# Performance work log

Hardware: AMD Instinct MI355X
Metric: run time of the kernel (lower is better)

## Reference

```python
import jax, jax.numpy as jnp
import numpy as np

D_MODEL = 768
N_HEADS = 8
Q_RANK = 64
KV_RANK = 64
ROPE_DIM = 64
NOPE_DIM = D_MODEL // N_HEADS - ROPE_DIM  # 32
V_DIM = D_MODEL // N_HEADS               # 96
Q_HEAD_DIM = NOPE_DIM + ROPE_DIM         # 96
EPS = 1e-6
ROPE_BASE = 10000.0


def rms_norm(x, w, eps=EPS):
    v = jnp.mean(jnp.square(x.astype(jnp.float32)), axis=-1, keepdims=True)
    return (x.astype(jnp.float32) * jax.lax.rsqrt(v + eps)).astype(x.dtype) * w


def rope_cos_sin(seq_len, dim):
    inv_freq = 1.0 / (ROPE_BASE ** (jnp.arange(0, dim, 2, dtype=jnp.float32) / dim))
    freqs = jnp.outer(jnp.arange(seq_len, dtype=jnp.float32), inv_freq)
    emb = jnp.concatenate([freqs, freqs], axis=-1)  # [s, dim]
    return jnp.cos(emb), jnp.sin(emb)


def apply_rope(x, cos, sin, pos_ids):
    # x: [b,h,s,d]; DeepSeek-V2 de-interleaves pairs before rotate_half
    b, h, s, d = x.shape
    x = x.reshape(b, h, s, d // 2, 2).transpose(0, 1, 2, 4, 3).reshape(b, h, s, d)
    c = cos[pos_ids][:, None]  # [b,1,s,d]
    sn = sin[pos_ids][:, None]
    x1, x2 = jnp.split(x, 2, axis=-1)
    rot = jnp.concatenate([-x2, x1], axis=-1)
    return x * c + rot * sn


def setup_inputs() -> dict:
    key = jax.random.key(0)
    ks = jax.random.split(key, 8)
    s = 0.02
    return {
        "src": jax.random.normal(ks[0], (4, 2048, D_MODEL), jnp.float32),
        "wq_a": jax.random.normal(ks[1], (Q_RANK, D_MODEL), jnp.float32) * s,
        "q_a_ln_w": jnp.ones((Q_RANK,), jnp.float32),
        "wq_b": jax.random.normal(ks[2], (N_HEADS * Q_HEAD_DIM, Q_RANK), jnp.float32) * s,
        "wkv_a": jax.random.normal(ks[3], (KV_RANK + ROPE_DIM, D_MODEL), jnp.float32) * s,
        "kv_a_ln_w": jnp.ones((KV_RANK,), jnp.float32),
        "wkv_b": jax.random.normal(ks[4], (N_HEADS * (NOPE_DIM + V_DIM), KV_RANK), jnp.float32) * s,
        "wo": jax.random.normal(ks[5], (D_MODEL, N_HEADS * V_DIM), jnp.float32) * s,
        "norm_w": jnp.ones((D_MODEL,), jnp.float32),
    }


def reference(src, wq_a, q_a_ln_w, wq_b, wkv_a, kv_a_ln_w, wkv_b, wo, norm_w):
    b, s, _ = src.shape
    pos = jnp.broadcast_to(jnp.arange(s)[None], (b, s))
    cos, sin = rope_cos_sin(s, ROPE_DIM)

    # ---- compress_kv (torch.no_grad in original) ----
    ckv = src @ wkv_a.T                                  # [b,s,rank+rope]
    c_lat, k_pe = ckv[..., :KV_RANK], ckv[..., KV_RANK:]
    c_lat = rms_norm(c_lat, kv_a_ln_w)
    k_pe = apply_rope(k_pe[:, None], cos, sin, pos)[:, 0]  # [b,s,rope]
    c_lat = jax.lax.stop_gradient(c_lat)
    k_pe = jax.lax.stop_gradient(k_pe)

    # ---- query path ----
    q = rms_norm(src @ wq_a.T, q_a_ln_w) @ wq_b.T        # [b,s,h*96]
    q = q.reshape(b, s, N_HEADS, Q_HEAD_DIM).transpose(0, 2, 1, 3)
    q_nope, q_pe = q[..., :NOPE_DIM], q[..., NOPE_DIM:]
    q_pe = apply_rope(q_pe, cos, sin, pos)

    # ---- absorb kv_b_proj ----
    w = wkv_b.reshape(N_HEADS, NOPE_DIM + V_DIM, KV_RANK)
    q_absorb, out_absorb = w[:, :NOPE_DIM], w[:, NOPE_DIM:]   # [h,32,r], [h,96,r]
    q_lat = jnp.einsum('bhsd,hdr->bhsr', q_nope, q_absorb)    # [b,h,s,r]

    scale = Q_HEAD_DIM ** -0.5
    scores = (jnp.einsum('bhsr,btr->bhst', q_lat, c_lat)
              + jnp.einsum('bhsd,btd->bhst', q_pe, k_pe)) * scale
    attn = jax.nn.softmax(scores.astype(jnp.float32), axis=-1).astype(src.dtype)

    ctx = jnp.einsum('bhst,btr->bhsr', attn, c_lat)           # [b,h,s,r]
    ctx = jnp.einsum('bhsr,hvr->bhsv', ctx, out_absorb)       # [b,h,s,96]
    attn_out = ctx.transpose(0, 2, 1, 3).reshape(b, s, N_HEADS * V_DIM) @ wo.T

    # residual (dropout in eval = identity) + RMSNorm
    return rms_norm(src + attn_out, norm_w)
```

## Files before the change

### kernel.cpp

```cpp
#include <hip/hip_runtime.h>


#define DEV static __device__ __forceinline__
typedef unsigned short ushort_t;
typedef __attribute__((ext_vector_type(8))) short bf8_t;
typedef __attribute__((ext_vector_type(4))) float f4_t;

DEV float bf2f(unsigned int u) {
    union { float f; unsigned int i; } x; x.i = u << 16; return x.f;
}
DEV ushort_t f2bf(float f) {
    union { float f; unsigned int u; } x; x.f = f;
    unsigned int u = x.u;
    return (ushort_t)((u + 0x7fffu + ((u >> 16) & 1u)) >> 16);
}
DEV float ldin(const void* p, size_t i, int isbf) {
    return isbf ? bf2f(((const ushort_t*)p)[i]) : ((const float*)p)[i];
}
DEV float fexp2(float x) {
#if __has_builtin(__builtin_amdgcn_exp2f)
    return __builtin_amdgcn_exp2f(x);
#else
    return exp2f(x);
#endif
}

constexpr int   TOK   = 4 * 2048;
constexpr float EPSF  = 1e-6f;
constexpr float QSCALE = (float)(0.10206207261596575 * 1.4426950408889634);
constexpr float L2_10000_OVER_32 = 0.4152410118609203f;

constexpr size_t OFF_WOT   = 0;
constexpr size_t OFF_WKVAT = 589824;
constexpr size_t OFF_WQAT  = 688128;
constexpr size_t OFF_WQBT  = 737280;
constexpr size_t OFF_QAF   = 786432;
constexpr size_t OFF_OAT   = 802816;
constexpr size_t OFF_QLN   = 851968;
constexpr size_t OFF_KVLN  = 852032;
constexpr size_t OFF_NW    = 852096;
constexpr size_t OFF_FLAG  = 852864;
constexpr size_t OFF_CTXF  = 852880;
constexpr size_t OFF_SRCBF = 3998608;
constexpr size_t OFF_KBF   = 7144336;
constexpr size_t OFF_VTB   = 7668624;
constexpr size_t OFF_QBF   = 7930768;
constexpr size_t OFF_ROPE  = 12125072;

__global__ void det_k(const unsigned int* __restrict__ nw_u, int* __restrict__ flag) {
    *flag = ((nw_u[0] & 0xffffu) != 0u) ? 1 : 0;
}

__global__ __launch_bounds__(256) void prep_k(
    const void* __restrict__ wq_a, const void* __restrict__ q_ln,
    const void* __restrict__ wq_b, const void* __restrict__ wkv_a,
    const void* __restrict__ kv_ln, const void* __restrict__ wkv_b,
    const void* __restrict__ wo, const void* __restrict__ nw,
    float* __restrict__ ws)
{
    const int isbf = ((const int*)ws)[OFF_FLAG];
    int i = blockIdx.x * 256 + threadIdx.x;
    int y = blockIdx.y;
    if (y == 0) {
        if (i < 768 * 768) {
            ushort_t* wob = (ushort_t*)(ws + OFF_WOT);
            wob[i] = isbf ? ((const ushort_t*)wo)[i] : f2bf(((const float*)wo)[i]);
        }
    } else if (y == 1) {
        if (i < 128 * 768) {
            ushort_t* d = (ushort_t*)(ws + OFF_WKVAT);
            d[i] = isbf ? ((const ushort_t*)wkv_a)[i] : f2bf(((const float*)wkv_a)[i]);
        }
    } else if (y == 2) {
        if (i < 64 * 768) {
            ushort_t* d = (ushort_t*)(ws + OFF_WQAT);
            d[i] = isbf ? ((const ushort_t*)wq_a)[i] : f2bf(((const float*)wq_a)[i]);
        }
    } else if (y == 3) {
        if (i < 768 * 64) {
            ushort_t* d = (ushort_t*)(ws + OFF_WQBT);
            d[i] = isbf ? ((const ushort_t*)wq_b)[i] : f2bf(((const float*)wq_b)[i]);
        }
    } else if (y == 4) {
        if (i < 8 * 64 * 32) {
            int h = i >> 11, rem = i & 2047, r = rem >> 5, d = rem & 31;
            ushort_t* dst = (ushort_t*)(ws + OFF_QAF);
            dst[i] = f2bf(ldin(wkv_b, (size_t)(h * 128 + d) * 64 + r, isbf) * QSCALE);
        }
    } else if (y == 5) {
        if (i < 8 * 64 * 96) {
            int h = i / 6144, rem = i - h * 6144;
            int r = rem / 96, v = rem - r * 96;
            ws[OFF_OAT + i] = ldin(wkv_b, (size_t)h * 8192 + 2048 + v * 64 + r, isbf);
        }
    } else if (y == 6) {
        if (i < 64)             ws[OFF_QLN + i]       = ldin(q_ln, i, isbf);
        else if (i < 128)       ws[OFF_KVLN + i - 64] = ldin(kv_ln, i - 64, isbf);
        else if (i < 128 + 768) ws[OFF_NW + i - 128]  = ldin(nw, i - 128, isbf);
    } else {
        if (i < 2048 * 32) {
            int pos = i >> 5, p = i & 31;
            float inv = exp2f(-(float)p * L2_10000_OVER_32);
            float ang = (float)pos * inv;
            float2* tab = (float2*)(ws + OFF_ROPE);
            tab[i] = make_float2(cosf(ang), sinf(ang));
        }
    }
}

__global__ __launch_bounds__(512) void k1_ckv(
    const void* __restrict__ src, const float* __restrict__ ws,
    ushort_t* __restrict__ Kbf, ushort_t* __restrict__ VTbf,
    ushort_t* __restrict__ srcbf)
{
    const ushort_t* wkvab = (const ushort_t*)(ws + OFF_WKVAT);
    const float* kvln  = ws + OFF_KVLN;
    const float2* tab  = (const float2*)(ws + OFF_ROPE);
    const int isbf = ((const int*)ws)[OFF_FLAG];
    __shared__ __align__(16) ushort_t sA[32 * 776];
    __shared__ float ckv[32][132];
    int j = threadIdx.x;
    int t0 = blockIdx.x * 32;
    int w = j >> 6, lane = j & 63;
    int tl = lane & 15, qd = lane >> 4;

    {
        for (int e = j; e < 32 * 96; e += 512) {
            int row = e / 96, c8 = e - row * 96;
            size_t off = (size_t)(t0 + row) * 768 + c8 * 8;
            if (isbf) {
                uint4 v = *(const uint4*)((const ushort_t*)src + off);
                *(uint4*)(sA + row * 776 + c8 * 8) = v;
            } else {
                const float4* p = (const float4*)((const float*)src + off);
                float4 f0 = p[0], f1 = p[1];
                ushort_t tmp[8] = {f2bf(f0.x), f2bf(f0.y), f2bf(f0.z), f2bf(f0.w),
                                   f2bf(f1.x), f2bf(f1.y), f2bf(f1.z), f2bf(f1.w)};
                uint4 v = *(const uint4*)tmp;
                *(uint4*)(sA + row * 776 + c8 * 8) = v;
                *(uint4*)(srcbf + off) = v;
            }
        }
    }
    __syncthreads();
    {
        f4_t acc[2];
        acc[0] = (f4_t){0.f, 0.f, 0.f, 0.f};
        acc[1] = (f4_t){0.f, 0.f, 0.f, 0.f};
        const ushort_t* bp = wkvab + (size_t)(w * 16 + tl) * 768 + qd * 8;
#pragma unroll 4
        for (int ks = 0; ks < 24; ++ks) {
            bf8_t b  = *(const bf8_t*)(bp + ks * 32);
            bf8_t a0 = *(const bf8_t*)(sA + tl * 776 + ks * 32 + qd * 8);
            bf8_t a1 = *(const bf8_t*)(sA + (16 + tl) * 776 + ks * 32 + qd * 8);
            acc[0] = __builtin_amdgcn_mfma_f32_16x16x32_bf16(a0, b, acc[0], 0, 0, 0);
            acc[1] = __builtin_amdgcn_mfma_f32_16x16x32_bf16(a1, b, acc[1], 0, 0, 0);
        }
#pragma unroll
        for (int mt = 0; mt < 2; ++mt)
#pragma unroll
            for (int r = 0; r < 4; ++r)
                ckv[mt * 16 + qd * 4 + r][w * 16 + tl] = acc[mt][r];
    }
    __syncthreads();

    if (j < 256) {
        int tt = j >> 3, l = j & 7;
        float ss = 0.f;
#pragma unroll
        for (int i = 0; i < 8; ++i) { float v = ckv[tt][l * 8 + i]; ss += v * v; }
        ss += __shfl_xor(ss, 1); ss += __shfl_xor(ss, 2); ss += __shfl_xor(ss, 4);
        float rs = rsqrtf(ss * (1.f / 64.f) + EPSF);
        size_t base = (size_t)(t0 + tt) * 128;
        ushort_t kb[8];
        float clw[8];
#pragma unroll
        for (int i = 0; i < 8; ++i) {
            int o2 = l * 8 + i;
            float cl = ckv[tt][o2] * rs;
            if (isbf) cl = bf2f(f2bf(cl));
            clw[i] = cl * kvln[o2];
            kb[i] = f2bf(clw[i]);
        }
        uint4 pack;
        pack.x = kb[0] | ((unsigned)kb[1] << 16); pack.y = kb[2] | ((unsigned)kb[3] << 16);
        pack.z = kb[4] | ((unsigned)kb[5] << 16); pack.w = kb[6] | ((unsigned)kb[7] << 16);
        *(uint4*)&Kbf[base + l * 8] = pack;
        int pos = (t0 + tt) & 2047;
        ushort_t r0[4], r1[4];
#pragma unroll
        for (int i = 0; i < 4; ++i) {
            int p = l * 4 + i;
            float2 cssn = tab[pos * 32 + p];
            float e = ckv[tt][64 + 2 * p], od = ckv[tt][64 + 2 * p + 1];
            r0[i] = f2bf(e * cssn.x - od * cssn.y);
            r1[i] = f2bf(od * cssn.x + e * cssn.y);
        }
        uint2 p0, p1;
        p0.x = r0[0] | ((unsigned)r0[1] << 16); p0.y = r0[2] | ((unsigned)r0[3] << 16);
        p1.x = r1[0] | ((unsigned)r1[1] << 16); p1.y = r1[2] | ((unsigned)r1[3] << 16);
        *(uint2*)&Kbf[base + 64 + l * 4] = p0;
        *(uint2*)&Kbf[base + 96 + l * 4] = p1;
#pragma unroll
        for (int i = 0; i < 8; ++i) ckv[tt][l * 8 + i] = clw[i];
    }
    __syncthreads();
    if (j < 256) {
        int t = j & 31, rb = (j >> 5) * 8;
        int bb = t0 >> 11, col = (t0 & 2047) + t;
#pragma unroll
        for (int i = 0; i < 8; ++i) {
            int r = rb + i;
            VTbf[((size_t)(bb * 64 + r)) * 2048 + col] = f2bf(ckv[t][r]);
        }
    }
}

__global__ __launch_bounds__(128) void k2_q(
    const void* __restrict__ src, const float* __restrict__ ws, ushort_t* __restrict__ Qbf)
{
    const int isbf = ((const int*)ws)[OFF_FLAG];
    const ushort_t* srcb = isbf ? (const ushort_t*)src : (const ushort_t*)(ws + OFF_SRCBF);
    const ushort_t* wqab = (const ushort_t*)(ws + OFF_WQAT);
    const ushort_t* wqbb = (const ushort_t*)(ws + OFF_WQBT);
    const ushort_t* qabs = (const ushort_t*)(ws + OFF_QAF);
    const float2*   tab  = (const float2*)(ws + OFF_ROPE);
    const float*    qln  = ws + OFF_QLN;

    __shared__ __align__(16) ushort_t LDS[2 * 3968];
    int j = threadIdx.x;
    int w = j >> 6, lane = j & 63;
    int tl = lane & 15, qd = lane >> 4;
    ushort_t* tmpn = LDS + w * 3968;
    ushort_t* qn   = tmpn + 1152;
    ushort_t* qf   = qn + 640;
    int tokw = blockIdx.x * 16;

    f4_t C1[4];
#pragma unroll
    for (int nt = 0; nt < 4; ++nt) C1[nt] = (f4_t){0.f, 0.f, 0.f, 0.f};
    {
        const ushort_t* ap = srcb + (size_t)(tokw + tl) * 768 + qd * 8;
#pragma unroll 4
        for (int ks = 0; ks < 24; ++ks) {
            bf8_t a = *(const bf8_t*)(ap + ks * 32);
#pragma unroll
            for (int nt = 0; nt < 4; ++nt) {
                bf8_t bfr = *(const bf8_t*)(wqab + (size_t)(nt * 16 + tl) * 768 + ks * 32 + qd * 8);
                C1[nt] = __builtin_amdgcn_mfma_f32_16x16x32_bf16(a, bfr, C1[nt], 0, 0, 0);
            }
        }
    }
    float rsv[4];
#pragma unroll
    for (int r = 0; r < 4; ++r) {
        float s = C1[0][r] * C1[0][r] + C1[1][r] * C1[1][r]
                + C1[2][r] * C1[2][r] + C1[3][r] * C1[3][r];
        s += __shfl_xor(s, 1); s += __shfl_xor(s, 2);
        s += __shfl_xor(s, 4); s += __shfl_xor(s, 8);
        rsv[r] = rsqrtf(s * (1.f / 64.f) + EPSF);
    }
    float qlnv[4];
#pragma unroll
    for (int nt = 0; nt < 4; ++nt) qlnv[nt] = qln[nt * 16 + tl];
#pragma unroll
    for (int nt = 0; nt < 4; ++nt)
#pragma unroll
        for (int r = 0; r < 4; ++r) {
            float v = C1[nt][r] * rsv[r];
            if (isbf) v = bf2f(f2bf(v));
            tmpn[(qd * 4 + r) * 72 + nt * 16 + tl] = f2bf(v * qlnv[nt]);
        }
    bf8_t A2[2];
#pragma unroll
    for (int ks = 0; ks < 2; ++ks) A2[ks] = *(const bf8_t*)(tmpn + tl * 72 + ks * 32 + qd * 8);

    float csv[4][4], snv[4][4];
#pragma unroll
    for (int nt2 = 0; nt2 < 4; ++nt2) {
        int p = (nt2 * 16 + tl) >> 1;
#pragma unroll
        for (int r = 0; r < 4; ++r) {
            int pos = (tokw + qd * 4 + r) & 2047;
            float2 t = tab[pos * 32 + p];
            csv[nt2][r] = t.x * QSCALE;
            snv[nt2][r] = t.y * QSCALE;
        }
    }
    const bool evn = !(tl & 1);
    int bb = tokw >> 11, pos0 = tokw & 2047;

    for (int h = w * 4; h < w * 4 + 4; ++h) {
        f4_t C2[6];
#pragma unroll
        for (int nt = 0; nt < 6; ++nt) C2[nt] = (f4_t){0.f, 0.f, 0.f, 0.f};
#pragma unroll
        for (int nt = 0; nt < 6; ++nt)
#pragma unroll
            for (int ks = 0; ks < 2; ++ks) {
                bf8_t bfr = *(const bf8_t*)(wqbb + (size_t)(h * 96 + nt * 16 + tl) * 64 + ks * 32 + qd * 8);
                C2[nt] = __builtin_amdgcn_mfma_f32_16x16x32_bf16(A2[ks], bfr, C2[nt], 0, 0, 0);
            }
#pragma unroll
        for (int nt = 0; nt < 2; ++nt)
#pragma unroll
            for (int r = 0; r < 4; ++r)
                qn[(qd * 4 + r) * 40 + nt * 16 + tl] = f2bf(C2[nt][r]);
        bf8_t an = *(const bf8_t*)(qn + tl * 40 + qd * 8);
        f4_t C3[4];
#pragma unroll
        for (int nt = 0; nt < 4; ++nt) C3[nt] = (f4_t){0.f, 0.f, 0.f, 0.f};
#pragma unroll
        for (int nt = 0; nt < 4; ++nt) {
            bf8_t bfr = *(const bf8_t*)(qabs + (size_t)h * 2048 + (nt * 16 + tl) * 32 + qd * 8);
            C3[nt] = __builtin_amdgcn_mfma_f32_16x16x32_bf16(an, bfr, C3[nt], 0, 0, 0);
        }
#pragma unroll
        for (int nt = 0; nt < 4; ++nt)
#pragma unroll
            for (int r = 0; r < 4; ++r)
                qf[(qd * 4 + r) * 136 + nt * 16 + tl] = f2bf(C3[nt][r]);
#pragma unroll
        for (int nt2 = 0; nt2 < 4; ++nt2) {
            int p = (nt2 * 16 + tl) >> 1;
            int outc = evn ? (64 + p) : (96 + p);
#pragma unroll
            for (int r = 0; r < 4; ++r) {
                float val = C2[nt2 + 2][r];
                float part = __shfl_xor(val, 1);
                float res = evn ? (val * csv[nt2][r] - part * snv[nt2][r])
                                : (val * csv[nt2][r] + part * snv[nt2][r]);
                qf[(qd * 4 + r) * 136 + outc] = f2bf(res);
            }
        }
        size_t qb = ((size_t)(bb * 8 + h) * 2048 + pos0) * 128;
#pragma unroll
        for (int i = 0; i < 4; ++i) {
            int idx = i * 64 + lane;
            int row = idx >> 4, c = idx & 15;
            uint4 v = *(const uint4*)(qf + row * 136 + c * 8);
            *(uint4*)(Qbf + qb + (size_t)row * 128 + c * 8) = v;
        }
    }
}

__global__ __launch_bounds__(256, 2) void k3_attn(
    const ushort_t* __restrict__ Qbf, const ushort_t* __restrict__ Kbf,
    const ushort_t* __restrict__ VTbf, const float* __restrict__ oaT,
    ushort_t* __restrict__ ctxb)
{
    __shared__ __align__(16) ushort_t LDS[22528];
    ushort_t* Kt = LDS;
    ushort_t* Vt = LDS + 8704;
    ushort_t* Pw = LDS + 13312;
    int j = threadIdx.x;
    int b = blockIdx.z, h = blockIdx.y, q0g = blockIdx.x * 128;
    int w = j >> 6, lane = j & 63;
    int tl = lane & 15, qd = lane >> 4;
    ushort_t* Pme = Pw + w * 2304;
    int qw = q0g + w * 32;

    bf8_t qfA[4], qfB[4];
    {
        const ushort_t* qp = Qbf + ((size_t)((b * 8 + h) * 2048) + qw + tl) * 128 + qd * 8;
#pragma unroll
        for (int ks = 0; ks < 4; ++ks) {
            qfA[ks] = *(const bf8_t*)(qp + ks * 32);
            qfB[ks] = *(const bf8_t*)(qp + 16 * 128 + ks * 32);
        }
    }
    f4_t OaccA[4], OaccB[4];
#pragma unroll
    for (int nt = 0; nt < 4; ++nt) {
        OaccA[nt] = (f4_t){0.f, 0.f, 0.f, 0.f};
        OaccB[nt] = (f4_t){0.f, 0.f, 0.f, 0.f};
    }
    float lA = 0.f, lB = 0.f;

    const size_t kbase = (size_t)b * 2048 * 128;
    const size_t vbase = (size_t)b * 64 * 2048;

    for (int it = 0; it < 32; ++it) {
        __syncthreads();
        {
            int r = j >> 2, c0 = (j & 3) * 32;
            const uint4* gp = (const uint4*)(Kbf + kbase + (size_t)(it * 64 + r) * 128 + c0);
            uint4 a0 = gp[0], a1 = gp[1], a2 = gp[2], a3 = gp[3];
            uint4* dp = (uint4*)(Kt + r * 136 + c0);
            dp[0] = a0; dp[1] = a1; dp[2] = a2; dp[3] = a3;
        }
        {
            int d = j >> 2, c0 = (j & 3) * 16;
            const uint4* gp = (const uint4*)(VTbf + vbase + (size_t)d * 2048 + it * 64 + c0);
            uint4 a0 = gp[0], a1 = gp[1];
            uint4* dp = (uint4*)(Vt + d * 72 + c0);
            dp[0] = a0; dp[1] = a1;
        }
        __syncthreads();
        f4_t SA[4], SB[4];
#pragma unroll
        for (int nt = 0; nt < 4; ++nt) {
            f4_t cA = (f4_t){0.f, 0.f, 0.f, 0.f};
            f4_t cB = (f4_t){0.f, 0.f, 0.f, 0.f};
#pragma unroll
            for (int ks = 0; ks < 4; ++ks) {
                bf8_t kf = *(const bf8_t*)(Kt + (nt * 16 + tl) * 136 + ks * 32 + qd * 8);
                cA = __builtin_amdgcn_mfma_f32_16x16x32_bf16(kf, qfA[ks], cA, 0, 0, 0);
                cB = __builtin_amdgcn_mfma_f32_16x16x32_bf16(kf, qfB[ks], cB, 0, 0, 0);
            }
            SA[nt] = cA; SB[nt] = cB;
        }
        float rsA = 0.f, rsB = 0.f;
#pragma unroll
        for (int nt = 0; nt < 4; ++nt)
#pragma unroll
            for (int r = 0; r < 4; ++r) {
                float pA = fexp2(SA[nt][r]); SA[nt][r] = pA; rsA += pA;
                float pB = fexp2(SB[nt][r]); SB[nt][r] = pB; rsB += pB;
            }
        rsA += __shfl_xor(rsA, 16); rsA += __shfl_xor(rsA, 32);
        rsB += __shfl_xor(rsB, 16); rsB += __shfl_xor(rsB, 32);
        lA += rsA; lB += rsB;
#pragma unroll
        for (int nt = 0; nt < 4; ++nt) {
            uint2 pkA, pkB;
            pkA.x = f2bf(SA[nt][0]) | ((unsigned)f2bf(SA[nt][1]) << 16);
            pkA.y = f2bf(SA[nt][2]) | ((unsigned)f2bf(SA[nt][3]) << 16);
            pkB.x = f2bf(SB[nt][0]) | ((unsigned)f2bf(SB[nt][1]) << 16);
            pkB.y = f2bf(SB[nt][2]) | ((unsigned)f2bf(SB[nt][3]) << 16);
            *(uint2*)(Pme + tl * 72 + nt * 16 + qd * 4) = pkA;
            *(uint2*)(Pme + (16 + tl) * 72 + nt * 16 + qd * 4) = pkB;
        }
        bf8_t pfA[2], pfB[2];
#pragma unroll
        for (int ks = 0; ks < 2; ++ks) {
            pfA[ks] = *(const bf8_t*)(Pme + tl * 72 + ks * 32 + qd * 8);
            pfB[ks] = *(const bf8_t*)(Pme + (16 + tl) * 72 + ks * 32 + qd * 8);
        }
#pragma unroll
        for (int nt = 0; nt < 4; ++nt)
#pragma unroll
            for (int ks = 0; ks < 2; ++ks) {
                bf8_t vf = *(const bf8_t*)(Vt + (nt * 16 + tl) * 72 + ks * 32 + qd * 8);
                OaccA[nt] = __builtin_amdgcn_mfma_f32_16x16x32_bf16(pfA[ks], vf, OaccA[nt], 0, 0, 0);
                OaccB[nt] = __builtin_amdgcn_mfma_f32_16x16x32_bf16(pfB[ks], vf, OaccB[nt], 0, 0, 0);
            }
    }
    {
        float linvA[4], linvB[4];
#pragma unroll
        for (int r = 0; r < 4; ++r) {
            float lqA = __shfl(lA, (lane & 48) + qd * 4 + r);
            float lqB = __shfl(lB, (lane & 48) + qd * 4 + r);
            linvA[r] = 1.f / lqA; linvB[r] = 1.f / lqB;
        }
#pragma unroll
        for (int nt = 0; nt < 4; ++nt)
#pragma unroll
            for (int r = 0; r < 4; ++r) {
                Pme[(qd * 4 + r) * 72 + nt * 16 + tl] = f2bf(OaccA[nt][r] * linvA[r]);
                Pme[(16 + qd * 4 + r) * 72 + nt * 16 + tl] = f2bf(OaccB[nt][r] * linvB[r]);
            }
    }
    __syncthreads();
    ushort_t* OA = LDS;
    for (int e = j; e < 96 * 64; e += 256) {
        int v = e >> 6, r = e & 63;
        OA[v * 72 + r] = f2bf(oaT[h * 6144 + r * 96 + v]);
    }
    __syncthreads();
    {
        bf8_t ofA[2], ofB[2];
#pragma unroll
        for (int ks = 0; ks < 2; ++ks) {
            ofA[ks] = *(const bf8_t*)(Pme + tl * 72 + ks * 32 + qd * 8);
            ofB[ks] = *(const bf8_t*)(Pme + (16 + tl) * 72 + ks * 32 + qd * 8);
        }
#pragma unroll
        for (int nt = 0; nt < 6; ++nt) {
            f4_t cA = (f4_t){0.f, 0.f, 0.f, 0.f};
            f4_t cB = (f4_t){0.f, 0.f, 0.f, 0.f};
#pragma unroll
            for (int ks = 0; ks < 2; ++ks) {
                bf8_t af = *(const bf8_t*)(OA + (nt * 16 + tl) * 72 + ks * 32 + qd * 8);
                cA = __builtin_amdgcn_mfma_f32_16x16x32_bf16(ofA[ks], af, cA, 0, 0, 0);
                cB = __builtin_amdgcn_mfma_f32_16x16x32_bf16(ofB[ks], af, cB, 0, 0, 0);
            }
#pragma unroll
            for (int r = 0; r < 4; ++r) {
                size_t tokA = (size_t)(b * 2048 + qw + qd * 4 + r);
                size_t tokB = tokA + 16;
                ctxb[tokA * 768 + h * 96 + nt * 16 + tl] = f2bf(cA[r]);
                ctxb[tokB * 768 + h * 96 + nt * 16 + tl] = f2bf(cB[r]);
            }
        }
    }
}

__global__ __launch_bounds__(256, 1) void k5_out(
    const void* __restrict__ src, const float* __restrict__ ws,
    const ushort_t* __restrict__ ctxb, void* __restrict__ out)
{
    const ushort_t* woB = (const ushort_t*)(ws + OFF_WOT);
    const float* nw = ws + OFF_NW;
    const int isbf = ((const int*)ws)[OFF_FLAG];
    __shared__ __align__(16) ushort_t ylds[32 * 776];
    int j = threadIdx.x;
    int t0 = blockIdx.x * 32;
    int w = j >> 6, lane = j & 63;
    int tl = lane & 15, qd = lane >> 4;
    int n0 = w * 192;

    {
        for (int e = j; e < 32 * 96; e += 256) {
            int row = e / 96, c16 = e - row * 96;
            uint4 v = *(const uint4*)(ctxb + (size_t)(t0 + row) * 768 + c16 * 8);
            *(uint4*)(ylds + row * 776 + c16 * 8) = v;
        }
    }
    __syncthreads();

    f4_t acc[2][12];
#pragma unroll
    for (int mt = 0; mt < 2; ++mt)
#pragma unroll
        for (int nt = 0; nt < 12; ++nt) acc[mt][nt] = (f4_t){0.f, 0.f, 0.f, 0.f};

#pragma unroll 2
    for (int ks = 0; ks < 24; ++ks) {
        bf8_t a0 = *(const bf8_t*)(ylds + tl * 776 + ks * 32 + qd * 8);
        bf8_t a1 = *(const bf8_t*)(ylds + (16 + tl) * 776 + ks * 32 + qd * 8);
#pragma unroll
        for (int nt = 0; nt < 12; ++nt) {
            bf8_t bfr = *(const bf8_t*)(woB + (size_t)(n0 + nt * 16 + tl) * 768 + ks * 32 + qd * 8);
            acc[0][nt] = __builtin_amdgcn_mfma_f32_16x16x32_bf16(a0, bfr, acc[0][nt], 0, 0, 0);
            acc[1][nt] = __builtin_amdgcn_mfma_f32_16x16x32_bf16(a1, bfr, acc[1][nt], 0, 0, 0);
        }
    }
    __syncthreads();

    {
#pragma unroll
        for (int mt = 0; mt < 2; ++mt)
#pragma unroll
            for (int nt = 0; nt < 12; ++nt)
#pragma unroll
                for (int r = 0; r < 4; ++r) {
                    int trow = mt * 16 + qd * 4 + r;
                    int col = n0 + nt * 16 + tl;
                    float yv = acc[mt][nt][r] + ldin(src, (size_t)(t0 + trow) * 768 + col, isbf);
                    ylds[trow * 776 + col] = f2bf(yv);
                }
    }
    __syncthreads();
    {
        int tt = j >> 3, sub = j & 7;
        const ushort_t* yp = ylds + tt * 776 + sub * 96;
        float ss = 0.f;
#pragma unroll
        for (int c = 0; c < 96; ++c) { float v = bf2f(yp[c]); ss += v * v; }
        ss += __shfl_xor(ss, 1); ss += __shfl_xor(ss, 2); ss += __shfl_xor(ss, 4);
        float rs = rsqrtf(ss * (1.f / 768.f) + EPSF);
        size_t base = (size_t)(t0 + tt) * 768 + sub * 96;
        if (isbf) {
            ushort_t* op = (ushort_t*)out + base;
#pragma unroll
            for (int c8 = 0; c8 < 12; ++c8) {
                ushort_t tmp[8];
#pragma unroll
                for (int c = 0; c < 8; ++c) {
                    float yv = bf2f(yp[c8 * 8 + c]);
                    float hv = bf2f(f2bf(yv * rs));
                    tmp[c] = f2bf(hv * nw[sub * 96 + c8 * 8 + c]);
                }
                *(uint4*)(op + c8 * 8) = *(const uint4*)tmp;
            }
        } else {
            float* op = (float*)out + base;
#pragma unroll
            for (int c = 0; c < 96; ++c) {
                float yv = bf2f(yp[c]);
                op[c] = yv * rs * nw[sub * 96 + c];
            }
        }
    }
}

extern "C" void kernel_launch(void* const* d_in, const int* in_sizes, int n_in,
                              void* d_out, int out_size, void* d_ws, size_t ws_size,
                              hipStream_t stream)
{
    const void* src   = d_in[0];
    const void* wq_a  = d_in[1];
    const void* q_ln  = d_in[2];
    const void* wq_b  = d_in[3];
    const void* wkv_a = d_in[4];
    const void* kv_ln = d_in[5];
    const void* wkv_b = d_in[6];
    const void* wo    = d_in[7];
    const void* nw    = d_in[8];
    float* ws = (float*)d_ws;
    ushort_t* Kbf   = (ushort_t*)(ws + OFF_KBF);
    ushort_t* VTbf  = (ushort_t*)(ws + OFF_VTB);
    ushort_t* Qbf   = (ushort_t*)(ws + OFF_QBF);
    ushort_t* ctxb  = (ushort_t*)(ws + OFF_CTXF);
    ushort_t* srcbf = (ushort_t*)(ws + OFF_SRCBF);

    det_k<<<dim3(1), dim3(1), 0, stream>>>((const unsigned int*)nw, (int*)ws + OFF_FLAG);
    prep_k<<<dim3(2304, 8), dim3(256), 0, stream>>>(wq_a, q_ln, wq_b, wkv_a, kv_ln, wkv_b, wo, nw, ws);
    k1_ckv<<<dim3(TOK / 32), dim3(512), 0, stream>>>(src, ws, Kbf, VTbf, srcbf);
    k2_q<<<dim3(TOK / 16), dim3(128), 0, stream>>>(src, ws, Qbf);
    k3_attn<<<dim3(16, 8, 4), dim3(256), 0, stream>>>(Qbf, Kbf, VTbf, ws + OFF_OAT, ctxb);
    k5_out<<<dim3(TOK / 32), dim3(256), 0, stream>>>(src, ws, ctxb, d_out);
}
```

Measured before the change: 304.6 us.

## Double-buffer K/V tiles in LDS with register prefetch in attention kernel

The attention kernel now keeps two LDS buffers for the K and V tiles and prefetches the tile two iterations ahead into registers. Each register-held tile is written to the other LDS buffer after the current compute, so each loop iteration needs one barrier instead of two and global load latency overlaps the MFMA work. s_setprio raises wave priority around the MFMA sections. This raises LDS use to about 70KB per block, which may still allow only two blocks per CU, and adds register pressure from the prefetch registers.

Result: slower. 349.1 us (+14.6%).

```diff
diff --git a/kernel.cpp b/kernel.cpp
--- a/kernel.cpp
+++ b/kernel.cpp
@@ -349,10 +349,8 @@
     const ushort_t* __restrict__ VTbf, const float* __restrict__ oaT,
     ushort_t* __restrict__ ctxb)
 {
-    __shared__ __align__(16) ushort_t LDS[22528];
-    ushort_t* Kt = LDS;
-    ushort_t* Vt = LDS + 8704;
-    ushort_t* Pw = LDS + 13312;
+    __shared__ __align__(16) ushort_t LDS[35840];
+    ushort_t* Pw = LDS + 26624;
     int j = threadIdx.x;
     int b = blockIdx.z, h = blockIdx.y, q0g = blockIdx.x * 128;
     int w = j >> 6, lane = j & 63;
@@ -380,24 +378,35 @@
     const size_t kbase = (size_t)b * 2048 * 128;
     const size_t vbase = (size_t)b * 64 * 2048;
 
+    const int srow = j >> 2;
+    const int kc0  = (j & 3) * 32;
+    const int vc0  = (j & 3) * 16;
+    const ushort_t* kgp = Kbf + kbase + (size_t)srow * 128 + kc0;
+    const ushort_t* vgp = VTbf + vbase + (size_t)srow * 2048 + vc0;
+
+    uint4 kr[4], vr[2];
+    {
+        const uint4* g  = (const uint4*)kgp;
+        kr[0] = g[0]; kr[1] = g[1]; kr[2] = g[2]; kr[3] = g[3];
+        const uint4* g2 = (const uint4*)vgp;
+        vr[0] = g2[0]; vr[1] = g2[1];
+        uint4* kd = (uint4*)(LDS + srow * 136 + kc0);
+        kd[0] = kr[0]; kd[1] = kr[1]; kd[2] = kr[2]; kd[3] = kr[3];
+        uint4* vd = (uint4*)(LDS + 17408 + srow * 72 + vc0);
+        vd[0] = vr[0]; vd[1] = vr[1];
+        const uint4* g3 = (const uint4*)(kgp + 64 * 128);
+        kr[0] = g3[0]; kr[1] = g3[1]; kr[2] = g3[2]; kr[3] = g3[3];
+        const uint4* g4 = (const uint4*)(vgp + 64);
+        vr[0] = g4[0]; vr[1] = g4[1];
+    }
+    __syncthreads();
+
     for (int it = 0; it < 32; ++it) {
-        __syncthreads();
-        {
-            int r = j >> 2, c0 = (j & 3) * 32;
-            const uint4* gp = (const uint4*)(Kbf + kbase + (size_t)(it * 64 + r) * 128 + c0);
-            uint4 a0 = gp[0], a1 = gp[1], a2 = gp[2], a3 = gp[3];
-            uint4* dp = (uint4*)(Kt + r * 136 + c0);
-            dp[0] = a0; dp[1] = a1; dp[2] = a2; dp[3] = a3;
-        }
-        {
-            int d = j >> 2, c0 = (j & 3) * 16;
-            const uint4* gp = (const uint4*)(VTbf + vbase + (size_t)d * 2048 + it * 64 + c0);
-            uint4 a0 = gp[0], a1 = gp[1];
-            uint4* dp = (uint4*)(Vt + d * 72 + c0);
-            dp[0] = a0; dp[1] = a1;
-        }
-        __syncthreads();
+        ushort_t* Kt = LDS + (it & 1) * 8704;
+        ushort_t* Vt = LDS + 17408 + (it & 1) * 4608;
+
         f4_t SA[4], SB[4];
+        __builtin_amdgcn_s_setprio(1);
 #pragma unroll
         for (int nt = 0; nt < 4; ++nt) {
             f4_t cA = (f4_t){0.f, 0.f, 0.f, 0.f};
@@ -410,6 +419,7 @@
             }
             SA[nt] = cA; SB[nt] = cB;
         }
+        __builtin_amdgcn_s_setprio(0);
         float rsA = 0.f, rsB = 0.f;
 #pragma unroll
         for (int nt = 0; nt < 4; ++nt)
@@ -437,6 +447,7 @@
             pfA[ks] = *(const bf8_t*)(Pme + tl * 72 + ks * 32 + qd * 8);
             pfB[ks] = *(const bf8_t*)(Pme + (16 + tl) * 72 + ks * 32 + qd * 8);
         }
+        __builtin_amdgcn_s_setprio(1);
 #pragma unroll
         for (int nt = 0; nt < 4; ++nt)
 #pragma unroll
@@ -445,6 +456,22 @@
                 OaccA[nt] = __builtin_amdgcn_mfma_f32_16x16x32_bf16(pfA[ks], vf, OaccA[nt], 0, 0, 0);
                 OaccB[nt] = __builtin_amdgcn_mfma_f32_16x16x32_bf16(pfB[ks], vf, OaccB[nt], 0, 0, 0);
             }
+        __builtin_amdgcn_s_setprio(0);
+
+        if (it < 31) {
+            int nb = (it + 1) & 1;
+            uint4* kd = (uint4*)(LDS + nb * 8704 + srow * 136 + kc0);
+            kd[0] = kr[0]; kd[1] = kr[1]; kd[2] = kr[2]; kd[3] = kr[3];
+            uint4* vd = (uint4*)(LDS + 17408 + nb * 4608 + srow * 72 + vc0);
+            vd[0] = vr[0]; vd[1] = vr[1];
+            if (it < 30) {
+                const uint4* g  = (const uint4*)(kgp + (size_t)(it + 2) * 64 * 128);
+                kr[0] = g[0]; kr[1] = g[1]; kr[2] = g[2]; kr[3] = g[3];
+                const uint4* g2 = (const uint4*)(vgp + (it + 2) * 64);
+                vr[0] = g2[0]; vr[1] = g2[1];
+            }
+        }
+        __syncthreads();
     }
     {
         float linvA[4], linvB[4];
@@ -476,6 +503,7 @@
             ofA[ks] = *(const bf8_t*)(Pme + tl * 72 + ks * 32 + qd * 8);
             ofB[ks] = *(const bf8_t*)(Pme + (16 + tl) * 72 + ks * 32 + qd * 8);
         }
+        __builtin_amdgcn_s_setprio(1);
 #pragma unroll
         for (int nt = 0; nt < 6; ++nt) {
             f4_t cA = (f4_t){0.f, 0.f, 0.f, 0.f};
@@ -494,6 +522,7 @@
                 ctxb[tokB * 768 + h * 96 + nt * 16 + tl] = f2bf(cB[r]);
             }
         }
+        __builtin_amdgcn_s_setprio(0);
     }
 }
 
```
